# Kernel optimization log

Measured on AMD Instinct MI355X. Metric: run time of the kernel, lower is better.

## Reference

```python
import jax, jax.numpy as jnp
import numpy as np

B = 16384
D_IN = 1024
D_OUT = 512
H1 = 4 * D_IN      # floor(layersDimentions[0]*inputDimention) = 4096
H3 = 4 * D_OUT     # floor(layersDimentions[1]*outputDimention) = 2048
H4 = 4 * D_OUT     # floor(layersDimentions[2]*outputDimention) = 2048
M = 256            # codebook size


def _linear_params(key, fan_in, fan_out):
    kw, kb = jax.random.split(key)
    bound = 1.0 / np.sqrt(fan_in)
    w = jax.random.uniform(kw, (fan_out, fan_in), jnp.float32, -bound, bound)
    b = jax.random.uniform(kb, (fan_out,), jnp.float32, -bound, bound)
    return w, b


def setup_inputs() -> dict:
    key = jax.random.key(0)
    ks = jax.random.split(key, 7)
    x = jax.random.normal(ks[0], (B, D_IN), jnp.float32)
    codebook = jnp.sort(jax.random.normal(ks[1], (M,), jnp.float32))
    w1, b1 = _linear_params(ks[2], D_IN, H1)
    w2, b2 = _linear_params(ks[3], H1, D_OUT)
    w3, b3 = _linear_params(ks[4], D_OUT, H3)
    w4, b4 = _linear_params(ks[5], H3, H4)
    w5, b5 = _linear_params(ks[6], H4, D_OUT)
    return {"x": x, "codebook": codebook,
            "w1": w1, "b1": b1, "w2": w2, "b2": b2,
            "w3": w3, "b3": b3, "w4": w4, "b4": b4,
            "w5": w5, "b5": b5}


def _quantize(x, codebook):
    # nearest codeword per scalar element: argmin_m |x - c_m|
    # x: [B, D], codebook: [M]
    d = jnp.abs(x[..., None] - codebook)          # [B, D, M]
    idx = jnp.argmin(d, axis=-1)                  # [B, D]
    return codebook[idx]


def reference(x, codebook, w1, b1, w2, b2, w3, b3, w4, b4, w5, b5):
    h = x @ w1.T + b1                # [B, H1]
    h = h @ w2.T + b2                # [B, D_OUT]
    h = _quantize(h, codebook)       # [B, D_OUT]
    h = h @ w3.T + b3                # [B, H3]
    h = h @ w4.T + b4                # [B, H4]
    return h @ w5.T + b5             # [B, D_OUT]
```

## Files before the change

kernel.cpp:

```cpp
#include <hip/hip_runtime.h>


typedef __bf16 v8bf __attribute__((ext_vector_type(8)));
typedef float  v4f  __attribute__((ext_vector_type(4)));

#define Bdim   16384
#define DIN    1024
#define DOUT   512
#define H1dim  4096
#define H3dim  2048
#define H4dim  2048

#define GLOBAL_AS __attribute__((address_space(1)))
#define LDS_AS    __attribute__((address_space(3)))

__device__ __forceinline__ void load16_to_lds(const __bf16* g, __bf16* l) {
  __builtin_amdgcn_global_load_lds((const GLOBAL_AS unsigned int*)g,
                                   (LDS_AS unsigned int*)l, 16, 0, 0);
}

__device__ __forceinline__ unsigned pack2bf(float a, float b) {
  return (unsigned)__builtin_bit_cast(unsigned short, (__bf16)a) |
         ((unsigned)__builtin_bit_cast(unsigned short, (__bf16)b) << 16);
}

__global__ void transpose_cast_kernel(const float* __restrict__ in,
                                      __bf16* __restrict__ out, int R, int C) {
  __shared__ float tile[32][33];
  const int c0 = blockIdx.x * 32, r0 = blockIdx.y * 32;
  const int t = threadIdx.x, tr = t >> 5, tc = t & 31;
#pragma unroll
  for (int i = 0; i < 4; ++i)
    tile[tr + i * 8][tc] = in[(size_t)(r0 + tr + i * 8) * C + (c0 + tc)];
  __syncthreads();
#pragma unroll
  for (int i = 0; i < 4; ++i)
    out[(size_t)(c0 + tr + i * 8) * R + (r0 + tc)] = (__bf16)tile[tc][tr + i * 8];
}

__global__ void bias_kernel(const float* __restrict__ b1, const float* __restrict__ w2,
                            const float* __restrict__ b2, const float* __restrict__ b3,
                            const __bf16* __restrict__ WtT, const float* __restrict__ b4,
                            const float* __restrict__ w5, const float* __restrict__ b5,
                            float* __restrict__ ba, float* __restrict__ bc) {
  const int wave = threadIdx.x >> 6, lane = threadIdx.x & 63;
  if (blockIdx.x < 128) {
    const int j = blockIdx.x * 4 + wave;
    float s = 0.f;
    for (int k = lane; k < H1dim; k += 64) s += b1[k] * w2[(size_t)j * H1dim + k];
#pragma unroll
    for (int off = 32; off; off >>= 1) s += __shfl_xor(s, off, 64);
    if (lane == 0) ba[j] = s + b2[j];
  } else {
    const int j = (blockIdx.x - 128) * 4 + wave;
    float s = 0.f;
    for (int k = lane; k < H4dim; k += 64)
      s += b3[k] * (float)WtT[(size_t)j * H4dim + k] + b4[k] * w5[(size_t)j * H4dim + k];
#pragma unroll
    for (int off = 32; off; off >>= 1) s += __shfl_xor(s, off, 64);
    if (lane == 0) bc[j] = s + b5[j];
  }
}

template <bool ABF16>
__global__ __launch_bounds__(256, 4)
void gemm_bt_splitk_kernel(const void* __restrict__ Ain, const __bf16* __restrict__ Bt,
                           float* __restrict__ Cpart, int M, int N, int K, int Kchunk) {
  __shared__ __bf16 As[64 * 32];
  __shared__ __bf16 Bs[64 * 32];
  const int t = threadIdx.x;
  const int m0 = blockIdx.x * 64;
  const int n0 = blockIdx.y * 64;
  const int kbeg = blockIdx.z * Kchunk;
  const int lane = t & 63, wave = t >> 6;
  const int quad = lane >> 4, l15 = lane & 15;
  const int wm = (wave & 1) * 32, wn = (wave >> 1) * 32;

  v4f acc[2][2];
#pragma unroll
  for (int i = 0; i < 2; ++i)
#pragma unroll
    for (int j = 0; j < 2; ++j) acc[i][j] = (v4f){0.f, 0.f, 0.f, 0.f};

  const int e = t * 8, r = e >> 5, c = e & 31;
  for (int k0 = kbeg; k0 < kbeg + Kchunk; k0 += 32) {
    if constexpr (ABF16) {
      const __bf16* A = (const __bf16*)Ain;
      *(int4*)&As[e] = *(const int4*)&A[(size_t)(m0 + r) * K + (k0 + c)];
    } else {
      const float* A = (const float*)Ain;
#pragma unroll
      for (int p = 0; p < 2; ++p) {
        const int idx = p * 256 + t;
        const int row = idx >> 3, col = (idx & 7) * 4;
        float4 v = *(const float4*)&A[(size_t)(m0 + row) * K + (k0 + col)];
        uint2 o;
        o.x = pack2bf(v.x, v.y);
        o.y = pack2bf(v.z, v.w);
        *(uint2*)&As[row * 32 + col] = o;
      }
    }
    *(int4*)&Bs[e] = *(const int4*)&Bt[(size_t)(n0 + r) * K + (k0 + c)];
    __syncthreads();
    v8bf af[2], bfr[2];
#pragma unroll
    for (int i = 0; i < 2; ++i) {
      af[i]  = *(const v8bf*)&As[(wm + i * 16 + l15) * 32 + quad * 8];
      bfr[i] = *(const v8bf*)&Bs[(wn + i * 16 + l15) * 32 + quad * 8];
    }
#pragma unroll
    for (int i = 0; i < 2; ++i)
#pragma unroll
      for (int j = 0; j < 2; ++j)
        acc[i][j] = __builtin_amdgcn_mfma_f32_16x16x32_bf16(af[i], bfr[j], acc[i][j], 0, 0, 0);
    __syncthreads();
  }

  float* dst = Cpart + (size_t)blockIdx.z * M * N;
#pragma unroll
  for (int i = 0; i < 2; ++i)
#pragma unroll
    for (int j = 0; j < 2; ++j)
#pragma unroll
      for (int r2 = 0; r2 < 4; ++r2) {
        const int gm = m0 + wm + i * 16 + quad * 4 + r2;
        const int gn = n0 + wn + j * 16 + l15;
        dst[(size_t)gm * N + gn] = acc[i][j][r2];
      }
}

__global__ void reduce_cast_kernel(const float* __restrict__ part,
                                   __bf16* __restrict__ out, int MN4, int S) {
  int i = blockIdx.x * blockDim.x + threadIdx.x;
  if (i >= MN4) return;
  const float4* p = reinterpret_cast<const float4*>(part);
  float4 s = p[i];
  for (int k = 1; k < S; ++k) {
    float4 v = p[(size_t)k * MN4 + i];
    s.x += v.x; s.y += v.y; s.z += v.z; s.w += v.w;
  }
  uint2 o;
  o.x = pack2bf(s.x, s.y);
  o.y = pack2bf(s.z, s.w);
  reinterpret_cast<uint2*>(out)[i] = o;
}

enum { MODE_Q = 1, MODE_OUT = 2 };

template <int MODE>
__global__ __launch_bounds__(256, 4)
void gemm_bt_kernel(const void* __restrict__ Ain, const __bf16* __restrict__ Bt,
                    void* __restrict__ Cout, const float* __restrict__ bias,
                    const float* __restrict__ codebook, int M, int N, int K) {
  __shared__ __bf16 As[128 * 32];
  __shared__ __bf16 Bs[64 * 32];
  __shared__ float cbs[256];

  const int t = threadIdx.x;
  const int m0 = blockIdx.x * 128;
  const int n0 = blockIdx.y * 64;
  if (MODE == MODE_Q) cbs[t] = codebook[t];

  const int lane = t & 63, wave = t >> 6;
  const int quad = lane >> 4, l15 = lane & 15;
  const int wm = (wave & 1) * 64, wn = (wave >> 1) * 32;

  const int srow = (lane >> 2);
  const int scol = (lane & 3) * 8;
  const __bf16* gB0 = Bt + (size_t)(n0 + 16 * wave + srow) * K + scol;
  __bf16* lB0 = &Bs[wave * 512];

  const __bf16* gA0 = nullptr;
  const __bf16* gA1 = nullptr;
  __bf16* lA0 = &As[wave * 512];
  __bf16* lA1 = &As[(wave + 4) * 512];
  if constexpr (MODE == MODE_OUT) {
    const __bf16* Ab = (const __bf16*)Ain;
    gA0 = Ab + (size_t)(m0 + 16 * wave + srow) * K + scol;
    gA1 = Ab + (size_t)(m0 + 64 + 16 * wave + srow) * K + scol;
  }
  const float* Af = (const float*)Ain;

  v4f acc[4][2];
#pragma unroll
  for (int i = 0; i < 4; ++i)
#pragma unroll
    for (int j = 0; j < 2; ++j) acc[i][j] = (v4f){0.f, 0.f, 0.f, 0.f};

  for (int k0 = 0; k0 < K; k0 += 32) {
    load16_to_lds(gB0 + k0, lB0);
    if constexpr (MODE == MODE_OUT) {
      load16_to_lds(gA0 + k0, lA0);
      load16_to_lds(gA1 + k0, lA1);
    } else {
#pragma unroll
      for (int p = 0; p < 4; ++p) {
        const int idx = p * 256 + t;
        const int row = idx >> 3, col = (idx & 7) * 4;
        float4 v = *(const float4*)&Af[(size_t)(m0 + row) * K + (k0 + col)];
        uint2 o;
        o.x = pack2bf(v.x, v.y);
        o.y = pack2bf(v.z, v.w);
        *(uint2*)&As[row * 32 + col] = o;
      }
    }
    __syncthreads();

    v8bf af[4], bfr[2];
#pragma unroll
    for (int i = 0; i < 4; ++i)
      af[i] = *(const v8bf*)&As[(wm + i * 16 + l15) * 32 + quad * 8];
#pragma unroll
    for (int j = 0; j < 2; ++j)
      bfr[j] = *(const v8bf*)&Bs[(wn + j * 16 + l15) * 32 + quad * 8];
#pragma unroll
    for (int i = 0; i < 4; ++i)
#pragma unroll
      for (int j = 0; j < 2; ++j)
        acc[i][j] = __builtin_amdgcn_mfma_f32_16x16x32_bf16(af[i], bfr[j], acc[i][j], 0, 0, 0);
    __syncthreads();
  }

#pragma unroll
  for (int i = 0; i < 4; ++i) {
#pragma unroll
    for (int j = 0; j < 2; ++j) {
#pragma unroll
      for (int r = 0; r < 4; ++r) {
        const int gm = m0 + wm + i * 16 + quad * 4 + r;
        const int gn = n0 + wn + j * 16 + l15;
        float v = acc[i][j][r];
        if constexpr (MODE == MODE_Q) {
          v += bias[gn];
          int idx = 0;
#pragma unroll
          for (int s = 128; s > 0; s >>= 1) {
            const int u = idx + s;
            if (cbs[u] <= v) idx = u;
          }
          float best = cbs[idx];
          if (idx < 255) {
            const float c1 = cbs[idx + 1];
            if (!(v - best <= c1 - v)) best = c1;
          }
          ((__bf16*)Cout)[(size_t)gm * N + gn] = (__bf16)best;
        } else {
          v += bias[gn];
          ((float*)Cout)[(size_t)gm * N + gn] = v;
        }
      }
    }
  }
}

extern "C" void kernel_launch(void* const* d_in, const int* in_sizes, int n_in,
                              void* d_out, int out_size, void* d_ws, size_t ws_size,
                              hipStream_t stream) {
  const float* x  = (const float*)d_in[0];
  const float* cb = (const float*)d_in[1];
  const float* w1 = (const float*)d_in[2];
  const float* b1 = (const float*)d_in[3];
  const float* w2 = (const float*)d_in[4];
  const float* b2 = (const float*)d_in[5];
  const float* w3 = (const float*)d_in[6];
  const float* b3 = (const float*)d_in[7];
  const float* w4 = (const float*)d_in[8];
  const float* b4 = (const float*)d_in[9];
  const float* w5 = (const float*)d_in[10];
  const float* b5 = (const float*)d_in[11];
  float* out = (float*)d_out;

  char* ws = (char*)d_ws;
  size_t off = 0;
  auto alloc = [&](size_t bytes) -> void* {
    void* p = ws + off;
    off = (off + bytes + 255) & ~(size_t)255;
    return p;
  };
  __bf16* w1T   = (__bf16*)alloc((size_t)DIN * H1dim * 2);
  __bf16* w4T   = (__bf16*)alloc((size_t)H3dim * H4dim * 2);
  __bf16* w3T   = (__bf16*)alloc((size_t)DOUT * H3dim * 2);
  __bf16* WaT   = (__bf16*)alloc((size_t)DOUT * DIN * 2);
  __bf16* WtT   = (__bf16*)alloc((size_t)DOUT * H3dim * 2);
  __bf16* WcT   = (__bf16*)alloc((size_t)DOUT * DOUT * 2);
  __bf16* q     = (__bf16*)alloc((size_t)Bdim * DOUT * 2);
  float*  ba    = (float*)alloc(DOUT * 4);
  float*  bc    = (float*)alloc(DOUT * 4);
  float*  part  = (float*)alloc((size_t)8 * DOUT * DIN * 4);

  transpose_cast_kernel<<<dim3(DIN / 32, H1dim / 32), 256, 0, stream>>>(w1, w1T, H1dim, DIN);
  transpose_cast_kernel<<<dim3(H3dim / 32, H4dim / 32), 256, 0, stream>>>(w4, w4T, H4dim, H3dim);
  transpose_cast_kernel<<<dim3(DOUT / 32, H3dim / 32), 256, 0, stream>>>(w3, w3T, H3dim, DOUT);

  gemm_bt_splitk_kernel<false><<<dim3(DOUT / 64, DIN / 64, 8), 256, 0, stream>>>(
      w2, w1T, part, DOUT, DIN, H1dim, H1dim / 8);
  reduce_cast_kernel<<<(DOUT * DIN / 4 + 255) / 256, 256, 0, stream>>>(
      part, WaT, DOUT * DIN / 4, 8);

  gemm_bt_splitk_kernel<false><<<dim3(DOUT / 64, H3dim / 64, 4), 256, 0, stream>>>(
      w5, w4T, part, DOUT, H3dim, H4dim, H4dim / 4);
  reduce_cast_kernel<<<(DOUT * H3dim / 4 + 255) / 256, 256, 0, stream>>>(
      part, WtT, DOUT * H3dim / 4, 4);

  bias_kernel<<<256, 256, 0, stream>>>(b1, w2, b2, b3, WtT, b4, w5, b5, ba, bc);

  gemm_bt_splitk_kernel<true><<<dim3(DOUT / 64, DOUT / 64, 8), 256, 0, stream>>>(
      WtT, w3T, part, DOUT, DOUT, H3dim, H3dim / 8);
  reduce_cast_kernel<<<(DOUT * DOUT / 4 + 255) / 256, 256, 0, stream>>>(
      part, WcT, DOUT * DOUT / 4, 8);

  gemm_bt_kernel<MODE_Q><<<dim3(Bdim / 128, DOUT / 64), 256, 0, stream>>>(
      x, WaT, q, ba, cb, Bdim, DOUT, DIN);
  gemm_bt_kernel<MODE_OUT><<<dim3(Bdim / 128, DOUT / 64), 256, 0, stream>>>(
      q, WcT, out, bc, nullptr, Bdim, DOUT, DOUT);
}
```

Baseline: 301.3 us.

## Merge prep kernels, pad LDS, and enlarge register-prefetched main GEMM tiles

The three weight transposes become one launch, the two independent split-K weight folds share a launch and a combined reduction, and the third fold is merged with the bias computation. The split-K LDS rows are padded from 32 to 40 elements to cut bank conflicts. The two batch GEMMs now use 128x128 tiles with K-step 64, padded LDS, and a register prefetch of the next K slab in place of the direct global-to-LDS loads. The intent is fewer launches and more MFMA work per LDS load, at the cost of higher register and LDS use and therefore lower occupancy.

```diff
diff --git a/kernel.cpp b/kernel.cpp
--- a/kernel.cpp
+++ b/kernel.cpp
@@ -11,23 +11,16 @@
 #define H3dim  2048
 #define H4dim  2048
 
-#define GLOBAL_AS __attribute__((address_space(1)))
-#define LDS_AS    __attribute__((address_space(3)))
-
-__device__ __forceinline__ void load16_to_lds(const __bf16* g, __bf16* l) {
-  __builtin_amdgcn_global_load_lds((const GLOBAL_AS unsigned int*)g,
-                                   (LDS_AS unsigned int*)l, 16, 0, 0);
-}
-
 __device__ __forceinline__ unsigned pack2bf(float a, float b) {
   return (unsigned)__builtin_bit_cast(unsigned short, (__bf16)a) |
          ((unsigned)__builtin_bit_cast(unsigned short, (__bf16)b) << 16);
 }
 
-__global__ void transpose_cast_kernel(const float* __restrict__ in,
-                                      __bf16* __restrict__ out, int R, int C) {
-  __shared__ float tile[32][33];
-  const int c0 = blockIdx.x * 32, r0 = blockIdx.y * 32;
+__device__ __forceinline__ void transpose_body(const float* __restrict__ in,
+                                               __bf16* __restrict__ out,
+                                               int R, int C, int bx, int by,
+                                               float (*tile)[33]) {
+  const int c0 = bx * 32, r0 = by * 32;
   const int t = threadIdx.x, tr = t >> 5, tc = t & 31;
 #pragma unroll
   for (int i = 0; i < 4; ++i)
@@ -38,21 +31,41 @@
     out[(size_t)(c0 + tr + i * 8) * R + (r0 + tc)] = (__bf16)tile[tc][tr + i * 8];
 }
 
-__global__ void bias_kernel(const float* __restrict__ b1, const float* __restrict__ w2,
-                            const float* __restrict__ b2, const float* __restrict__ b3,
-                            const __bf16* __restrict__ WtT, const float* __restrict__ b4,
-                            const float* __restrict__ w5, const float* __restrict__ b5,
-                            float* __restrict__ ba, float* __restrict__ bc) {
+__global__ void transpose3_kernel(const float* __restrict__ w1, __bf16* __restrict__ w1T,
+                                  const float* __restrict__ w4, __bf16* __restrict__ w4T,
+                                  const float* __restrict__ w3, __bf16* __restrict__ w3T) {
+  __shared__ float tile[32][33];
+  int b = blockIdx.x;
+  if (b < 4096) {
+    transpose_body(w1, w1T, H1dim, DIN, b & 31, b >> 5, tile);
+  } else if (b < 8192) {
+    b -= 4096;
+    transpose_body(w4, w4T, H4dim, H3dim, b & 63, b >> 6, tile);
+  } else {
+    b -= 8192;
+    transpose_body(w3, w3T, H3dim, DOUT, b & 15, b >> 4, tile);
+  }
+}
+
+__device__ __forceinline__ void bias_body(int bb, const float* __restrict__ b1,
+                                          const float* __restrict__ w2,
+                                          const float* __restrict__ b2,
+                                          const float* __restrict__ b3,
+                                          const __bf16* __restrict__ WtT,
+                                          const float* __restrict__ b4,
+                                          const float* __restrict__ w5,
+                                          const float* __restrict__ b5,
+                                          float* __restrict__ ba, float* __restrict__ bc) {
   const int wave = threadIdx.x >> 6, lane = threadIdx.x & 63;
-  if (blockIdx.x < 128) {
-    const int j = blockIdx.x * 4 + wave;
+  if (bb < 128) {
+    const int j = bb * 4 + wave;
     float s = 0.f;
     for (int k = lane; k < H1dim; k += 64) s += b1[k] * w2[(size_t)j * H1dim + k];
 #pragma unroll
     for (int off = 32; off; off >>= 1) s += __shfl_xor(s, off, 64);
     if (lane == 0) ba[j] = s + b2[j];
   } else {
-    const int j = (blockIdx.x - 128) * 4 + wave;
+    const int j = (bb - 128) * 4 + wave;
     float s = 0.f;
     for (int k = lane; k < H4dim; k += 64)
       s += b3[k] * (float)WtT[(size_t)j * H4dim + k] + b4[k] * w5[(size_t)j * H4dim + k];
@@ -63,15 +76,15 @@
 }
 
 template <bool ABF16>
-__global__ __launch_bounds__(256, 4)
-void gemm_bt_splitk_kernel(const void* __restrict__ Ain, const __bf16* __restrict__ Bt,
-                           float* __restrict__ Cpart, int M, int N, int K, int Kchunk) {
-  __shared__ __bf16 As[64 * 32];
-  __shared__ __bf16 Bs[64 * 32];
+__device__ __forceinline__ void splitk_body(__bf16* As, __bf16* Bs,
+                                            int bx, int by, int bz,
+                                            const void* __restrict__ Ain,
+                                            const __bf16* __restrict__ Bt,
+                                            float* __restrict__ Cpart,
+                                            int M, int N, int K, int Kchunk) {
   const int t = threadIdx.x;
-  const int m0 = blockIdx.x * 64;
-  const int n0 = blockIdx.y * 64;
-  const int kbeg = blockIdx.z * Kchunk;
+  const int m0 = bx * 64, n0 = by * 64;
+  const int kbeg = bz * Kchunk;
   const int lane = t & 63, wave = t >> 6;
   const int quad = lane >> 4, l15 = lane & 15;
   const int wm = (wave & 1) * 32, wn = (wave >> 1) * 32;
@@ -82,11 +95,11 @@
 #pragma unroll
     for (int j = 0; j < 2; ++j) acc[i][j] = (v4f){0.f, 0.f, 0.f, 0.f};
 
-  const int e = t * 8, r = e >> 5, c = e & 31;
+  const int r = t >> 2, c = (t & 3) * 8;
   for (int k0 = kbeg; k0 < kbeg + Kchunk; k0 += 32) {
     if constexpr (ABF16) {
       const __bf16* A = (const __bf16*)Ain;
-      *(int4*)&As[e] = *(const int4*)&A[(size_t)(m0 + r) * K + (k0 + c)];
+      *(int4*)&As[r * 40 + c] = *(const int4*)&A[(size_t)(m0 + r) * K + (k0 + c)];
     } else {
       const float* A = (const float*)Ain;
 #pragma unroll
@@ -97,16 +110,16 @@
         uint2 o;
         o.x = pack2bf(v.x, v.y);
         o.y = pack2bf(v.z, v.w);
-        *(uint2*)&As[row * 32 + col] = o;
+        *(uint2*)&As[row * 40 + col] = o;
       }
     }
-    *(int4*)&Bs[e] = *(const int4*)&Bt[(size_t)(n0 + r) * K + (k0 + c)];
+    *(int4*)&Bs[r * 40 + c] = *(const int4*)&Bt[(size_t)(n0 + r) * K + (k0 + c)];
     __syncthreads();
     v8bf af[2], bfr[2];
 #pragma unroll
     for (int i = 0; i < 2; ++i) {
-      af[i]  = *(const v8bf*)&As[(wm + i * 16 + l15) * 32 + quad * 8];
-      bfr[i] = *(const v8bf*)&Bs[(wn + i * 16 + l15) * 32 + quad * 8];
+      af[i]  = *(const v8bf*)&As[(wm + i * 16 + l15) * 40 + quad * 8];
+      bfr[i] = *(const v8bf*)&Bs[(wn + i * 16 + l15) * 40 + quad * 8];
     }
 #pragma unroll
     for (int i = 0; i < 2; ++i)
@@ -116,7 +129,7 @@
     __syncthreads();
   }
 
-  float* dst = Cpart + (size_t)blockIdx.z * M * N;
+  float* dst = Cpart + (size_t)bz * M * N;
 #pragma unroll
   for (int i = 0; i < 2; ++i)
 #pragma unroll
@@ -129,9 +142,45 @@
       }
 }
 
-__global__ void reduce_cast_kernel(const float* __restrict__ part,
-                                   __bf16* __restrict__ out, int MN4, int S) {
-  int i = blockIdx.x * blockDim.x + threadIdx.x;
+__global__ __launch_bounds__(256, 4)
+void fold12_kernel(const float* __restrict__ w2, const __bf16* __restrict__ w1T,
+                   float* __restrict__ part1,
+                   const float* __restrict__ w5, const __bf16* __restrict__ w4T,
+                   float* __restrict__ part2) {
+  __shared__ __align__(16) __bf16 As[64 * 40];
+  __shared__ __align__(16) __bf16 Bs[64 * 40];
+  int b = blockIdx.x;
+  if (b < 1024) {
+    splitk_body<false>(As, Bs, b & 7, (b >> 3) & 15, b >> 7,
+                       w2, w1T, part1, DOUT, DIN, H1dim, H1dim / 8);
+  } else {
+    b -= 1024;
+    splitk_body<false>(As, Bs, b & 7, (b >> 3) & 31, b >> 8,
+                       w5, w4T, part2, DOUT, H3dim, H4dim, H4dim / 4);
+  }
+}
+
+__global__ __launch_bounds__(256, 4)
+void fold3_bias_kernel(const __bf16* __restrict__ WtT, const __bf16* __restrict__ w3T,
+                       float* __restrict__ part,
+                       const float* __restrict__ b1, const float* __restrict__ w2,
+                       const float* __restrict__ b2, const float* __restrict__ b3,
+                       const float* __restrict__ b4, const float* __restrict__ w5,
+                       const float* __restrict__ b5,
+                       float* __restrict__ ba, float* __restrict__ bc) {
+  __shared__ __align__(16) __bf16 As[64 * 40];
+  __shared__ __align__(16) __bf16 Bs[64 * 40];
+  int b = blockIdx.x;
+  if (b < 512) {
+    splitk_body<true>(As, Bs, b & 7, (b >> 3) & 7, b >> 6,
+                      WtT, w3T, part, DOUT, DOUT, H3dim, H3dim / 8);
+  } else {
+    bias_body(b - 512, b1, w2, b2, b3, WtT, b4, w5, b5, ba, bc);
+  }
+}
+
+__device__ __forceinline__ void reduce_body(const float* __restrict__ part,
+                                            __bf16* __restrict__ out, int MN4, int S, int i) {
   if (i >= MN4) return;
   const float4* p = reinterpret_cast<const float4*>(part);
   float4 s = p[i];
@@ -145,93 +194,121 @@
   reinterpret_cast<uint2*>(out)[i] = o;
 }
 
+__global__ void reduce12_kernel(const float* __restrict__ part1, __bf16* __restrict__ WaT,
+                                const float* __restrict__ part2, __bf16* __restrict__ WtT) {
+  const int b = blockIdx.x, t = threadIdx.x;
+  if (b < 512) reduce_body(part1, WaT, DOUT * DIN / 4, 8, b * 256 + t);
+  else         reduce_body(part2, WtT, DOUT * H3dim / 4, 4, (b - 512) * 256 + t);
+}
+
+__global__ void reduce_cast_kernel(const float* __restrict__ part,
+                                   __bf16* __restrict__ out, int MN4, int S) {
+  int i = blockIdx.x * blockDim.x + threadIdx.x;
+  reduce_body(part, out, MN4, S, i);
+}
+
 enum { MODE_Q = 1, MODE_OUT = 2 };
 
 template <int MODE>
-__global__ __launch_bounds__(256, 4)
-void gemm_bt_kernel(const void* __restrict__ Ain, const __bf16* __restrict__ Bt,
-                    void* __restrict__ Cout, const float* __restrict__ bias,
-                    const float* __restrict__ codebook, int M, int N, int K) {
-  __shared__ __bf16 As[128 * 32];
-  __shared__ __bf16 Bs[64 * 32];
+__global__ __launch_bounds__(256)
+void gemm_main_kernel(const void* __restrict__ Ain, const __bf16* __restrict__ Bt,
+                      void* __restrict__ Cout, const float* __restrict__ bias,
+                      const float* __restrict__ codebook, int M, int N, int K) {
+  __shared__ __align__(16) __bf16 As[128 * 72];
+  __shared__ __align__(16) __bf16 Bs[128 * 72];
   __shared__ float cbs[256];
 
   const int t = threadIdx.x;
   const int m0 = blockIdx.x * 128;
-  const int n0 = blockIdx.y * 64;
-  if (MODE == MODE_Q) cbs[t] = codebook[t];
+  const int n0 = blockIdx.y * 128;
+  if constexpr (MODE == MODE_Q) cbs[t] = codebook[t];
 
   const int lane = t & 63, wave = t >> 6;
   const int quad = lane >> 4, l15 = lane & 15;
-  const int wm = (wave & 1) * 64, wn = (wave >> 1) * 32;
-
-  const int srow = (lane >> 2);
-  const int scol = (lane & 3) * 8;
-  const __bf16* gB0 = Bt + (size_t)(n0 + 16 * wave + srow) * K + scol;
-  __bf16* lB0 = &Bs[wave * 512];
-
-  const __bf16* gA0 = nullptr;
-  const __bf16* gA1 = nullptr;
-  __bf16* lA0 = &As[wave * 512];
-  __bf16* lA1 = &As[(wave + 4) * 512];
-  if constexpr (MODE == MODE_OUT) {
-    const __bf16* Ab = (const __bf16*)Ain;
-    gA0 = Ab + (size_t)(m0 + 16 * wave + srow) * K + scol;
-    gA1 = Ab + (size_t)(m0 + 64 + 16 * wave + srow) * K + scol;
-  }
-  const float* Af = (const float*)Ain;
-
-  v4f acc[4][2];
+  const int wm = (wave & 1) * 64, wn = (wave >> 1) * 64;
+
+  const float*  Af = (const float*)Ain;
+  const __bf16* Ab = (const __bf16*)Ain;
+
+  const int frow = t >> 4, fcol = (t & 15) * 4;
+  const int hrow = t >> 3, hcol = (t & 7) * 8;
+
+  float4 pa[8];
+  int4   pab[4];
+  int4   pb[4];
+
+  auto prefetch = [&](int k0) {
+    if constexpr (MODE == MODE_Q) {
+#pragma unroll
+      for (int p = 0; p < 8; ++p)
+        pa[p] = *(const float4*)&Af[(size_t)(m0 + p * 16 + frow) * K + (k0 + fcol)];
+    } else {
+#pragma unroll
+      for (int p = 0; p < 4; ++p)
+        pab[p] = *(const int4*)&Ab[(size_t)(m0 + p * 32 + hrow) * K + (k0 + hcol)];
+    }
+#pragma unroll
+    for (int p = 0; p < 4; ++p)
+      pb[p] = *(const int4*)&Bt[(size_t)(n0 + p * 32 + hrow) * K + (k0 + hcol)];
+  };
+  auto writelds = [&]() {
+    if constexpr (MODE == MODE_Q) {
+#pragma unroll
+      for (int p = 0; p < 8; ++p) {
+        uint2 o;
+        o.x = pack2bf(pa[p].x, pa[p].y);
+        o.y = pack2bf(pa[p].z, pa[p].w);
+        *(uint2*)&As[(p * 16 + frow) * 72 + fcol] = o;
+      }
+    } else {
+#pragma unroll
+      for (int p = 0; p < 4; ++p)
+        *(int4*)&As[(p * 32 + hrow) * 72 + hcol] = pab[p];
+    }
+#pragma unroll
+    for (int p = 0; p < 4; ++p)
+      *(int4*)&Bs[(p * 32 + hrow) * 72 + hcol] = pb[p];
+  };
+
+  v4f acc[4][4];
 #pragma unroll
   for (int i = 0; i < 4; ++i)
 #pragma unroll
-    for (int j = 0; j < 2; ++j) acc[i][j] = (v4f){0.f, 0.f, 0.f, 0.f};
-
-  for (int k0 = 0; k0 < K; k0 += 32) {
-    load16_to_lds(gB0 + k0, lB0);
-    if constexpr (MODE == MODE_OUT) {
-      load16_to_lds(gA0 + k0, lA0);
-      load16_to_lds(gA1 + k0, lA1);
-    } else {
-#pragma unroll
-      for (int p = 0; p < 4; ++p) {
-        const int idx = p * 256 + t;
-        const int row = idx >> 3, col = (idx & 7) * 4;
-        float4 v = *(const float4*)&Af[(size_t)(m0 + row) * K + (k0 + col)];
-        uint2 o;
-        o.x = pack2bf(v.x, v.y);
-        o.y = pack2bf(v.z, v.w);
-        *(uint2*)&As[row * 32 + col] = o;
-      }
-    }
+    for (int j = 0; j < 4; ++j) acc[i][j] = (v4f){0.f, 0.f, 0.f, 0.f};
+
+  prefetch(0);
+  for (int k0 = 0; k0 < K; k0 += 64) {
+    writelds();
     __syncthreads();
-
-    v8bf af[4], bfr[2];
-#pragma unroll
-    for (int i = 0; i < 4; ++i)
-      af[i] = *(const v8bf*)&As[(wm + i * 16 + l15) * 32 + quad * 8];
-#pragma unroll
-    for (int j = 0; j < 2; ++j)
-      bfr[j] = *(const v8bf*)&Bs[(wn + j * 16 + l15) * 32 + quad * 8];
-#pragma unroll
-    for (int i = 0; i < 4; ++i)
-#pragma unroll
-      for (int j = 0; j < 2; ++j)
-        acc[i][j] = __builtin_amdgcn_mfma_f32_16x16x32_bf16(af[i], bfr[j], acc[i][j], 0, 0, 0);
+    if (k0 + 64 < K) prefetch(k0 + 64);
+#pragma unroll
+    for (int kk = 0; kk < 2; ++kk) {
+      v8bf af[4], bv[4];
+#pragma unroll
+      for (int i = 0; i < 4; ++i)
+        af[i] = *(const v8bf*)&As[(wm + i * 16 + l15) * 72 + kk * 32 + quad * 8];
+#pragma unroll
+      for (int j = 0; j < 4; ++j)
+        bv[j] = *(const v8bf*)&Bs[(wn + j * 16 + l15) * 72 + kk * 32 + quad * 8];
+#pragma unroll
+      for (int i = 0; i < 4; ++i)
+#pragma unroll
+        for (int j = 0; j < 4; ++j)
+          acc[i][j] = __builtin_amdgcn_mfma_f32_16x16x32_bf16(af[i], bv[j], acc[i][j], 0, 0, 0);
+    }
     __syncthreads();
   }
 
 #pragma unroll
   for (int i = 0; i < 4; ++i) {
 #pragma unroll
-    for (int j = 0; j < 2; ++j) {
+    for (int j = 0; j < 4; ++j) {
 #pragma unroll
       for (int r = 0; r < 4; ++r) {
         const int gm = m0 + wm + i * 16 + quad * 4 + r;
         const int gn = n0 + wn + j * 16 + l15;
-        float v = acc[i][j][r];
+        float v = acc[i][j][r] + bias[gn];
         if constexpr (MODE == MODE_Q) {
-          v += bias[gn];
           int idx = 0;
 #pragma unroll
           for (int s = 128; s > 0; s >>= 1) {
@@ -245,7 +322,6 @@
           }
           ((__bf16*)Cout)[(size_t)gm * N + gn] = (__bf16)best;
         } else {
-          v += bias[gn];
           ((float*)Cout)[(size_t)gm * N + gn] = v;
         }
       }
@@ -277,40 +353,32 @@
     off = (off + bytes + 255) & ~(size_t)255;
     return p;
   };
-  __bf16* w1T   = (__bf16*)alloc((size_t)DIN * H1dim * 2);
-  __bf16* w4T   = (__bf16*)alloc((size_t)H3dim * H4dim * 2);
-  __bf16* w3T   = (__bf16*)alloc((size_t)DOUT * H3dim * 2);
-  __bf16* WaT   = (__bf16*)alloc((size_t)DOUT * DIN * 2);
-  __bf16* WtT   = (__bf16*)alloc((size_t)DOUT * H3dim * 2);
-  __bf16* WcT   = (__bf16*)alloc((size_t)DOUT * DOUT * 2);
-  __bf16* q     = (__bf16*)alloc((size_t)Bdim * DOUT * 2);
-  float*  ba    = (float*)alloc(DOUT * 4);
-  float*  bc    = (float*)alloc(DOUT * 4);
-  float*  part  = (float*)alloc((size_t)8 * DOUT * DIN * 4);
-
-  transpose_cast_kernel<<<dim3(DIN / 32, H1dim / 32), 256, 0, stream>>>(w1, w1T, H1dim, DIN);
-  transpose_cast_kernel<<<dim3(H3dim / 32, H4dim / 32), 256, 0, stream>>>(w4, w4T, H4dim, H3dim);
-  transpose_cast_kernel<<<dim3(DOUT / 32, H3dim / 32), 256, 0, stream>>>(w3, w3T, H3dim, DOUT);
-
-  gemm_bt_splitk_kernel<false><<<dim3(DOUT / 64, DIN / 64, 8), 256, 0, stream>>>(
-      w2, w1T, part, DOUT, DIN, H1dim, H1dim / 8);
-  reduce_cast_kernel<<<(DOUT * DIN / 4 + 255) / 256, 256, 0, stream>>>(
-      part, WaT, DOUT * DIN / 4, 8);
-
-  gemm_bt_splitk_kernel<false><<<dim3(DOUT / 64, H3dim / 64, 4), 256, 0, stream>>>(
-      w5, w4T, part, DOUT, H3dim, H4dim, H4dim / 4);
-  reduce_cast_kernel<<<(DOUT * H3dim / 4 + 255) / 256, 256, 0, stream>>>(
-      part, WtT, DOUT * H3dim / 4, 4);
-
-  bias_kernel<<<256, 256, 0, stream>>>(b1, w2, b2, b3, WtT, b4, w5, b5, ba, bc);
-
-  gemm_bt_splitk_kernel<true><<<dim3(DOUT / 64, DOUT / 64, 8), 256, 0, stream>>>(
-      WtT, w3T, part, DOUT, DOUT, H3dim, H3dim / 8);
-  reduce_cast_kernel<<<(DOUT * DOUT / 4 + 255) / 256, 256, 0, stream>>>(
-      part, WcT, DOUT * DOUT / 4, 8);
-
-  gemm_bt_kernel<MODE_Q><<<dim3(Bdim / 128, DOUT / 64), 256, 0, stream>>>(
+  __bf16* w1T  = (__bf16*)alloc((size_t)DIN * H1dim * 2);
+  __bf16* w4T  = (__bf16*)alloc((size_t)H3dim * H4dim * 2);
+  __bf16* w3T  = (__bf16*)alloc((size_t)DOUT * H3dim * 2);
+  __bf16* WaT  = (__bf16*)alloc((size_t)DOUT * DIN * 2);
+  __bf16* WtT  = (__bf16*)alloc((size_t)DOUT * H3dim * 2);
+  __bf16* WcT  = (__bf16*)alloc((size_t)DOUT * DOUT * 2);
+  __bf16* q    = (__bf16*)alloc((size_t)Bdim * DOUT * 2);
+  float*  ba   = (float*)alloc(DOUT * 4);
+  float*  bc   = (float*)alloc(DOUT * 4);
+  float*  part1 = (float*)alloc((size_t)8 * DOUT * DIN * 4);
+  float*  part2 = (float*)q;
+
+  transpose3_kernel<<<9216, 256, 0, stream>>>(w1, w1T, w4, w4T, w3, w3T);
+
+  fold12_kernel<<<2048, 256, 0, stream>>>(w2, w1T, part1, w5, w4T, part2);
+
+  reduce12_kernel<<<1536, 256, 0, stream>>>(part1, WaT, part2, WtT);
+
+  fold3_bias_kernel<<<768, 256, 0, stream>>>(WtT, w3T, part1,
+                                             b1, w2, b2, b3, b4, w5, b5, ba, bc);
+
+  reduce_cast_kernel<<<256, 256, 0, stream>>>(part1, WcT, DOUT * DOUT / 4, 8);
+
+  gemm_main_kernel<MODE_Q><<<dim3(Bdim / 128, DOUT / 128), 256, 0, stream>>>(
       x, WaT, q, ba, cb, Bdim, DOUT, DIN);
-  gemm_bt_kernel<MODE_OUT><<<dim3(Bdim / 128, DOUT / 64), 256, 0, stream>>>(
+
+  gemm_main_kernel<MODE_OUT><<<dim3(Bdim / 128, DOUT / 128), 256, 0, stream>>>(
       q, WcT, out, bc, nullptr, Bdim, DOUT, DOUT);
 }
```

Measured after the change: 357.4 us. 1.19x slower.
